# Performance work log

Hardware: AMD Instinct MI355X
Metric: run time of the kernel (lower is better)

The kernel has to match this reference:

```python
import jax, jax.numpy as jnp
import numpy as np

B, S, NS, MAX_W, H, NH = 4, 512, 8192, 16, 256, 4
DH = H // NH
FF = 4 * H
NEG = -1e9  # finite mask value; fully-padded spans are zeroed at the end anyway


def _layernorm(x, g, b, eps=1e-5):
    m = jnp.mean(x, -1, keepdims=True)
    v = jnp.var(x, -1, keepdims=True)
    return (x - m) * jax.lax.rsqrt(v + eps) * g + b


def _pos_encoding(n, d):
    pos = np.arange(n)[:, None]
    div = np.exp(np.arange(0, d, 2) * (-np.log(10000.0) / d))
    pe = np.zeros((n, d), np.float32)
    pe[:, 0::2] = np.sin(pos * div)
    pe[:, 1::2] = np.cos(pos * div)
    return jnp.asarray(pe)


def setup_inputs():
    key = jax.random.key(0)
    ks = jax.random.split(key, 12)
    sc = 1.0 / np.sqrt(H)
    starts = jax.random.randint(ks[1], (B, NS), 0, S - MAX_W)
    lengths = jax.random.randint(ks[2], (B, NS), 1, MAX_W + 1)
    return {
        "token_reps": jax.random.normal(ks[0], (B, S, H), jnp.float32),
        "span_ids": jnp.stack([starts, starts + lengths], -1),
        "span_masks": jax.random.uniform(ks[3], (B, NS)) < 0.9,
        "pooling": 1,
        "dummy_query": jax.random.normal(ks[4], (H,), jnp.float32) * sc,
        "w_q": jax.random.normal(ks[5], (H, H), jnp.float32) * sc,
        "w_k": jax.random.normal(ks[6], (H, H), jnp.float32) * sc,
        "w_v": jax.random.normal(ks[7], (H, H), jnp.float32) * sc,
        "b_qkv": jnp.zeros((3, H), jnp.float32),
        "w_o": jax.random.normal(ks[8], (H, H), jnp.float32) * sc,
        "b_o": jnp.zeros((H,), jnp.float32),
        "ln_g": jnp.ones((H,), jnp.float32),
        "ln_b": jnp.zeros((H,), jnp.float32),
        "ffn_w1": jax.random.normal(ks[9], (H, FF), jnp.float32) * sc,
        "ffn_b1": jnp.zeros((FF,), jnp.float32),
        "ffn_w2": jax.random.normal(ks[10], (FF, H), jnp.float32) * (1.0 / np.sqrt(FF)),
        "ffn_b2": jnp.zeros((H,), jnp.float32),
    }


def reference(token_reps, span_ids, span_masks, pooling, dummy_query, w_q, w_k, w_v,
              b_qkv, w_o, b_o, ln_g, ln_b, ffn_w1, ffn_b1, ffn_w2, ffn_b2):
    # sequence positional encoding (eval mode -> dropout is identity)
    tr = token_reps + _pos_encoding(S, H)[None]  # [B,S,H]
    # span lengths, zeroed where span is masked out (as in torch code)
    span_len = (span_ids[:, :, 1] - span_ids[:, :, 0]) * span_masks.astype(span_ids.dtype)  # [B,NS]
    offs = jnp.arange(MAX_W)
    valid = offs[None, None, :] < span_len[:, :, None]  # [B,NS,W] True = real token
    pos = jnp.clip(span_ids[:, :, 0:1] + offs[None, None, :], 0, S - 1)  # [B,NS,W]
    # vectorized ragged gather replacing the python double loop
    x = tr[jnp.arange(B)[:, None, None], pos]  # [B,NS,W,H]
    x = jnp.where(valid[..., None], x, 0.0)
    # single-query multi-head cross attention (dummy query attends over span tokens)
    q = (dummy_query @ w_q.T + b_qkv[0]).reshape(NH, DH)
    k = (x @ w_k.T + b_qkv[1]).reshape(B, NS, MAX_W, NH, DH)
    v = (x @ w_v.T + b_qkv[2]).reshape(B, NS, MAX_W, NH, DH)
    logits = jnp.einsum('hd,bnwhd->bnhw', q, k) / np.sqrt(DH)
    logits = jnp.where(valid[:, :, None, :], logits, NEG)
    attn = jax.nn.softmax(logits, axis=-1)
    ctx = jnp.einsum('bnhw,bnwhd->bnhd', attn, v).reshape(B, NS, H)
    out = ctx @ w_o.T + b_o + dummy_query  # residual with the dummy query
    y = _layernorm(out, ln_g, ln_b)
    f = jax.nn.relu(y @ ffn_w1 + ffn_b1) @ ffn_w2 + ffn_b2
    y = _layernorm(f + y, ln_g, ln_b)
    return jnp.where(span_masks[..., None], y, 0.0)  # [B,NS,H]
```

## Files before the change

kernel.cpp:

```cpp
#include <hip/hip_runtime.h>
#include <hip/hip_bf16.h>

#define B_    4
#define S_    512
#define NS_   8192
#define MAXW  16
#define H_    256
#define NH_   4
#define DH_   64
#define FF_   1024
#define NSPAN (B_*NS_)
#define NEGV  (-1.0e9f)
#define MT    64

typedef short s16x8 __attribute__((ext_vector_type(8)));
typedef float f32x4 __attribute__((ext_vector_type(4)));

__device__ __forceinline__ unsigned short f2bu(float v){
  __hip_bfloat16 h = __float2bfloat16(v);
  union { __hip_bfloat16 h; unsigned short u; } c; c.h = h; return c.u;
}
__device__ __forceinline__ float bu2f(unsigned short u){
  union { unsigned int i; float f; } c; c.i = ((unsigned int)u) << 16; return c.f;
}

__global__ void prep_tr_kernel(const float* __restrict__ tok,
                               float* __restrict__ tr,
                               unsigned short* __restrict__ trbf){
  int idx = blockIdx.x * 256 + threadIdx.x;
  int j = idx & (H_ - 1);
  int p = (idx >> 8) & (S_ - 1);
  float fac = expf((float)((j >> 1) * 2) * (-9.210340371976184f / 256.0f));
  float ang = (float)p * fac;
  float pe = (j & 1) ? cosf(ang) : sinf(ang);
  float v = tok[idx] + pe;
  tr[idx] = v;
  trbf[idx] = f2bu(v);
}

__global__ void prep_q_kernel(const float* __restrict__ dq,
                              const float* __restrict__ wq,
                              const float* __restrict__ wk,
                              const float* __restrict__ bqkv,
                              float* __restrict__ qkvec,
                              float* __restrict__ qb){
  __shared__ float q_s[H_];
  const int t = threadIdx.x;
  const int l = t & 63;
  const int wv = t >> 6;
  const int h = blockIdx.x;
  float4 dqv = *(const float4*)(dq + l*4);
  for (int r = 0; r < 64; ++r) {
    const int row = wv*64 + r;
    float4 wr = *(const float4*)(wq + (size_t)row*H_ + l*4);
    float p = wr.x*dqv.x + wr.y*dqv.y + wr.z*dqv.z + wr.w*dqv.w;
    p += __shfl_xor(p, 1);  p += __shfl_xor(p, 2);
    p += __shfl_xor(p, 4);  p += __shfl_xor(p, 8);
    p += __shfl_xor(p, 16); p += __shfl_xor(p, 32);
    if (l == 0) q_s[row] = p + bqkv[row];
  }
  __syncthreads();
  float s = 0.f;
  #pragma unroll 8
  for (int d = 0; d < DH_; ++d) s += q_s[h*DH_ + d] * wk[(h*DH_ + d)*H_ + t];
  qkvec[h*H_ + t] = s;
  if (t < 64) {
    float p = q_s[h*DH_ + t] * bqkv[H_ + h*DH_ + t];
    for (int off = 32; off; off >>= 1) p += __shfl_down(p, off);
    if (t == 0) qb[h] = p;
  }
}

__global__ __launch_bounds__(256) void prep_logit_kernel(
    const float* __restrict__ tr, const float* __restrict__ qkvec,
    const float* __restrict__ qb, float* __restrict__ lt)
{
  const int t = threadIdx.x, l = t & 63, wv = t >> 6;
  const int row = blockIdx.x * 4 + wv;
  float4 x = *(const float4*)(tr + (size_t)row*H_ + l*4);
  float p0, p1, p2, p3;
  {
    float4 q0 = *(const float4*)(qkvec + 0*H_ + l*4);
    float4 q1 = *(const float4*)(qkvec + 1*H_ + l*4);
    float4 q2 = *(const float4*)(qkvec + 2*H_ + l*4);
    float4 q3 = *(const float4*)(qkvec + 3*H_ + l*4);
    p0 = q0.x*x.x + q0.y*x.y + q0.z*x.z + q0.w*x.w;
    p1 = q1.x*x.x + q1.y*x.y + q1.z*x.z + q1.w*x.w;
    p2 = q2.x*x.x + q2.y*x.y + q2.z*x.z + q2.w*x.w;
    p3 = q3.x*x.x + q3.y*x.y + q3.z*x.z + q3.w*x.w;
  }
  #pragma unroll
  for (int m = 1; m < 64; m <<= 1) {
    p0 += __shfl_xor(p0, m); p1 += __shfl_xor(p1, m);
    p2 += __shfl_xor(p2, m); p3 += __shfl_xor(p3, m);
  }
  if (l < 4) {
    float pv = (l == 0) ? p0 : (l == 1) ? p1 : (l == 2) ? p2 : p3;
    lt[row*NH_ + l] = (pv + qb[l]) * 0.125f;
  }
}

__global__ void cast_bf16_kernel(const float* __restrict__ src,
                                 unsigned short* __restrict__ dst){
  int idx = blockIdx.x * 256 + threadIdx.x;
  dst[idx] = f2bu(src[idx]);
}

__global__ void prep_w1t_kernel(const float* __restrict__ w1,
                                unsigned short* __restrict__ w1t){
  int idx = blockIdx.x * 256 + threadIdx.x;
  int n = idx >> 8, k = idx & 255;
  w1t[idx] = f2bu(w1[k*FF_ + n]);
}
__global__ void prep_w2t_kernel(const float* __restrict__ w2,
                                unsigned short* __restrict__ w2t){
  int idx = blockIdx.x * 256 + threadIdx.x;
  int n = idx >> 10, k = idx & 1023;
  w2t[idx] = f2bu(w2[k*H_ + n]);
}

__global__ __launch_bounds__(256) void pool_kernel(
    const unsigned short* __restrict__ trbf,
    const float* __restrict__ lt,
    const int* __restrict__ span_ids, const int* __restrict__ span_masks,
    int span0, unsigned short* __restrict__ pooled)
{
  const int t = threadIdx.x;
  const int l = t & 63;
  const int wv = t >> 6;
  const int spanL = blockIdx.x * 4 + wv;
  const int span  = span0 + spanL;
  const int b  = span >> 13;
  const int st = span_ids[span*2];
  const int en = span_ids[span*2 + 1];
  const int len = span_masks[span] ? (en - st) : 0;

  const int h = l >> 4, w = l & 15;
  int pos = st + w; pos = pos < 0 ? 0 : (pos > S_-1 ? S_-1 : pos);
  float logit = (w < len) ? lt[(b*S_ + pos)*NH_ + h] : NEGV;
  float mx = logit;
  mx = fmaxf(mx, __shfl_xor(mx, 1));
  mx = fmaxf(mx, __shfl_xor(mx, 2));
  mx = fmaxf(mx, __shfl_xor(mx, 4));
  mx = fmaxf(mx, __shfl_xor(mx, 8));
  float e = expf(logit - mx);
  float se = e;
  se += __shfl_xor(se, 1); se += __shfl_xor(se, 2);
  se += __shfl_xor(se, 4); se += __shfl_xor(se, 8);
  const float av = e / se;

  float acc[NH_][4];
  #pragma unroll
  for (int hh = 0; hh < NH_; ++hh)
    #pragma unroll
    for (int j = 0; j < 4; ++j) acc[hh][j] = 0.f;

  const unsigned short* rb = trbf + (size_t)(b*S_)*H_ + l*4;
  #pragma unroll
  for (int w2 = 0; w2 < MAXW; ++w2) {
    int p2 = st + w2; p2 = p2 < 0 ? 0 : (p2 > S_-1 ? S_-1 : p2);
    ushort4 xv = *(const ushort4*)(rb + (size_t)p2*H_);
    float x0 = bu2f(xv.x), x1 = bu2f(xv.y), x2 = bu2f(xv.z), x3 = bu2f(xv.w);
    #pragma unroll
    for (int hh = 0; hh < NH_; ++hh) {
      float a = __shfl(av, hh*16 + w2);
      acc[hh][0] += a*x0; acc[hh][1] += a*x1;
      acc[hh][2] += a*x2; acc[hh][3] += a*x3;
    }
  }
  unsigned short* pp = pooled + (size_t)spanL * 1024;
  #pragma unroll
  for (int hh = 0; hh < NH_; ++hh) {
    ushort4 o;
    o.x = f2bu(acc[hh][0]); o.y = f2bu(acc[hh][1]);
    o.z = f2bu(acc[hh][2]); o.w = f2bu(acc[hh][3]);
    *(ushort4*)(pp + hh*256 + l*4) = o;
  }
}

template <typename AF>
__device__ __forceinline__ void do_gemm(AF aload, const unsigned short* __restrict__ bmat,
                                        int bstr, int koff, f32x4 (&ac)[4][4],
                                        int w, int ln16, int lg)
{
  s16x8 BA[4], BB[4];
  const unsigned short* bb = bmat + koff + lg*8;
  #pragma unroll
  for (int nf = 0; nf < 4; ++nf) {
    const unsigned short* bp = bb + (size_t)(w*64 + nf*16 + ln16)*bstr;
    BA[nf] = *(const s16x8*)bp;
    BB[nf] = *(const s16x8*)(bp + 32);
  }
  #pragma unroll
  for (int kk = 0; kk < 4; ++kk) {
    const int k0 = kk*64;
    {
      s16x8 a0 = aload(0*16 + ln16, k0 + lg*8);
      s16x8 a1 = aload(1*16 + ln16, k0 + lg*8);
      s16x8 a2 = aload(2*16 + ln16, k0 + lg*8);
      s16x8 a3 = aload(3*16 + ln16, k0 + lg*8);
      #pragma unroll
      for (int nf = 0; nf < 4; ++nf) {
        ac[0][nf] = __builtin_amdgcn_mfma_f32_16x16x32_bf16(a0, BA[nf], ac[0][nf], 0,0,0);
        ac[1][nf] = __builtin_amdgcn_mfma_f32_16x16x32_bf16(a1, BA[nf], ac[1][nf], 0,0,0);
        ac[2][nf] = __builtin_amdgcn_mfma_f32_16x16x32_bf16(a2, BA[nf], ac[2][nf], 0,0,0);
        ac[3][nf] = __builtin_amdgcn_mfma_f32_16x16x32_bf16(a3, BA[nf], ac[3][nf], 0,0,0);
      }
    }
    if (kk < 3) {
      #pragma unroll
      for (int nf = 0; nf < 4; ++nf)
        BA[nf] = *(const s16x8*)(bb + (size_t)(w*64 + nf*16 + ln16)*bstr + k0 + 64);
    }
    {
      s16x8 a0 = aload(0*16 + ln16, k0 + 32 + lg*8);
      s16x8 a1 = aload(1*16 + ln16, k0 + 32 + lg*8);
      s16x8 a2 = aload(2*16 + ln16, k0 + 32 + lg*8);
      s16x8 a3 = aload(3*16 + ln16, k0 + 32 + lg*8);
      #pragma unroll
      for (int nf = 0; nf < 4; ++nf) {
        ac[0][nf] = __builtin_amdgcn_mfma_f32_16x16x32_bf16(a0, BB[nf], ac[0][nf], 0,0,0);
        ac[1][nf] = __builtin_amdgcn_mfma_f32_16x16x32_bf16(a1, BB[nf], ac[1][nf], 0,0,0);
        ac[2][nf] = __builtin_amdgcn_mfma_f32_16x16x32_bf16(a2, BB[nf], ac[2][nf], 0,0,0);
        ac[3][nf] = __builtin_amdgcn_mfma_f32_16x16x32_bf16(a3, BB[nf], ac[3][nf], 0,0,0);
      }
    }
    if (kk < 3) {
      #pragma unroll
      for (int nf = 0; nf < 4; ++nf)
        BB[nf] = *(const s16x8*)(bb + (size_t)(w*64 + nf*16 + ln16)*bstr + k0 + 96);
    }
  }
}

__global__ __launch_bounds__(256) void fused_gemm_kernel(
    const unsigned short* __restrict__ pooled,
    const unsigned short* __restrict__ wvt,
    const unsigned short* __restrict__ wot,
    const float* __restrict__ bqkv, const float* __restrict__ bo,
    const float* __restrict__ dq,
    const unsigned short* __restrict__ w1t, const float* __restrict__ b1,
    const unsigned short* __restrict__ w2t, const float* __restrict__ b2,
    const float* __restrict__ lng, const float* __restrict__ lnb,
    const int* __restrict__ masks, int span0,
    float* __restrict__ out)
{
  __shared__ __align__(16) unsigned short buf_s[MT][264];
  __shared__ __align__(16) unsigned short y_s[MT][264];
  __shared__ float part_s[4][MT][2];

  const int t = threadIdx.x;
  const int l = t & 63;
  const int w = t >> 6;
  const int ln16 = l & 15;
  const int lg = l >> 4;
  const int m0l = blockIdx.x * MT;
  const int m0g = span0 + m0l;

  auto aldP = [&](int r, int kc) -> s16x8 {
    return *(const s16x8*)(pooled + (size_t)(m0l + r)*1024 + w*256 + kc);
  };
  auto aldY = [&](int r, int kc) -> s16x8 { return *(const s16x8*)&y_s[r][kc]; };
  auto aldB = [&](int r, int kc) -> s16x8 { return *(const s16x8*)&buf_s[r][kc]; };

  f32x4 acc[4][4];

  #pragma unroll
  for (int mf = 0; mf < 4; ++mf)
    #pragma unroll
    for (int nf = 0; nf < 4; ++nf) acc[mf][nf] = (f32x4){0.f,0.f,0.f,0.f};
  do_gemm(aldP, wvt, 256, 0, acc, w, ln16, lg);
  #pragma unroll
  for (int nf = 0; nf < 4; ++nf) {
    const int col = w*64 + nf*16 + ln16;
    const float bvv = bqkv[2*H_ + col];
    #pragma unroll
    for (int mf = 0; mf < 4; ++mf)
      #pragma unroll
      for (int r = 0; r < 4; ++r)
        buf_s[mf*16 + lg*4 + r][col] = f2bu(acc[mf][nf][r] + bvv);
  }
  __syncthreads();

  #pragma unroll
  for (int mf = 0; mf < 4; ++mf)
    #pragma unroll
    for (int nf = 0; nf < 4; ++nf) acc[mf][nf] = (f32x4){0.f,0.f,0.f,0.f};
  do_gemm(aldB, wot, 256, 0, acc, w, ln16, lg);

  {
    float bbv[4], glv[4], blv[4];
    #pragma unroll
    for (int nf = 0; nf < 4; ++nf) {
      const int col = w*64 + nf*16 + ln16;
      bbv[nf] = bo[col] + dq[col];
      glv[nf] = lng[col]; blv[nf] = lnb[col];
    }
    float vals[4][4][4];
    #pragma unroll
    for (int mf = 0; mf < 4; ++mf)
      #pragma unroll
      for (int r = 0; r < 4; ++r) {
        const int row = mf*16 + lg*4 + r;
        float s1 = 0.f, s2 = 0.f;
        #pragma unroll
        for (int nf = 0; nf < 4; ++nf) {
          float v = acc[mf][nf][r] + bbv[nf];
          vals[mf][r][nf] = v; s1 += v; s2 += v*v;
        }
        s1 += __shfl_xor(s1,1); s2 += __shfl_xor(s2,1);
        s1 += __shfl_xor(s1,2); s2 += __shfl_xor(s2,2);
        s1 += __shfl_xor(s1,4); s2 += __shfl_xor(s2,4);
        s1 += __shfl_xor(s1,8); s2 += __shfl_xor(s2,8);
        if (ln16 == 0) { part_s[w][row][0] = s1; part_s[w][row][1] = s2; }
      }
    __syncthreads();
    #pragma unroll
    for (int mf = 0; mf < 4; ++mf)
      #pragma unroll
      for (int r = 0; r < 4; ++r) {
        const int row = mf*16 + lg*4 + r;
        float s1 = part_s[0][row][0]+part_s[1][row][0]+part_s[2][row][0]+part_s[3][row][0];
        float s2 = part_s[0][row][1]+part_s[1][row][1]+part_s[2][row][1]+part_s[3][row][1];
        float mean = s1 * (1.f/H_);
        float var  = s2 * (1.f/H_) - mean*mean; var = fmaxf(var, 0.f);
        float rstd = rsqrtf(var + 1e-5f);
        #pragma unroll
        for (int nf = 0; nf < 4; ++nf) {
          const int col = w*64 + nf*16 + ln16;
          y_s[row][col] = f2bu((vals[mf][r][nf] - mean)*rstd*glv[nf] + blv[nf]);
        }
      }
  }
  __syncthreads();

  f32x4 f2acc[4][4];
  #pragma unroll
  for (int mf = 0; mf < 4; ++mf)
    #pragma unroll
    for (int nf = 0; nf < 4; ++nf) f2acc[mf][nf] = (f32x4){0.f,0.f,0.f,0.f};

  for (int nc = 0; nc < 4; ++nc) {
    #pragma unroll
    for (int mf = 0; mf < 4; ++mf)
      #pragma unroll
      for (int nf = 0; nf < 4; ++nf) acc[mf][nf] = (f32x4){0.f,0.f,0.f,0.f};
    do_gemm(aldY, w1t + nc*256*H_, 256, 0, acc, w, ln16, lg);
    __syncthreads();
    #pragma unroll
    for (int nf = 0; nf < 4; ++nf) {
      float bb = b1[nc*256 + w*64 + nf*16 + ln16];
      #pragma unroll
      for (int mf = 0; mf < 4; ++mf)
        #pragma unroll
        for (int r = 0; r < 4; ++r)
          buf_s[mf*16 + lg*4 + r][w*64 + nf*16 + ln16] = f2bu(fmaxf(acc[mf][nf][r] + bb, 0.f));
    }
    __syncthreads();
    do_gemm(aldB, w2t, 1024, nc*256, f2acc, w, ln16, lg);
  }

  float b2v[4], gv[4], bvv[4];
  #pragma unroll
  for (int nf = 0; nf < 4; ++nf) {
    const int col = w*64 + nf*16 + ln16;
    b2v[nf] = b2[col]; gv[nf] = lng[col]; bvv[nf] = lnb[col];
  }
  float vals[4][4][4];
  #pragma unroll
  for (int mf = 0; mf < 4; ++mf)
    #pragma unroll
    for (int r = 0; r < 4; ++r) {
      const int row = mf*16 + lg*4 + r;
      float s1 = 0.f, s2 = 0.f;
      #pragma unroll
      for (int nf = 0; nf < 4; ++nf) {
        float resid = bu2f(y_s[row][w*64 + nf*16 + ln16]);
        float v = f2acc[mf][nf][r] + b2v[nf] + resid;
        vals[mf][r][nf] = v; s1 += v; s2 += v*v;
      }
      s1 += __shfl_xor(s1,1); s2 += __shfl_xor(s2,1);
      s1 += __shfl_xor(s1,2); s2 += __shfl_xor(s2,2);
      s1 += __shfl_xor(s1,4); s2 += __shfl_xor(s2,4);
      s1 += __shfl_xor(s1,8); s2 += __shfl_xor(s2,8);
      if (ln16 == 0) { part_s[w][row][0] = s1; part_s[w][row][1] = s2; }
    }
  __syncthreads();
  #pragma unroll
  for (int mf = 0; mf < 4; ++mf)
    #pragma unroll
    for (int r = 0; r < 4; ++r) {
      const int row = mf*16 + lg*4 + r;
      const int span = m0g + row;
      float s1 = part_s[0][row][0]+part_s[1][row][0]+part_s[2][row][0]+part_s[3][row][0];
      float s2 = part_s[0][row][1]+part_s[1][row][1]+part_s[2][row][1]+part_s[3][row][1];
      float mean = s1 * (1.f/H_);
      float var  = s2 * (1.f/H_) - mean*mean; var = fmaxf(var, 0.f);
      float rstd = rsqrtf(var + 1e-5f);
      int mk = masks[span];
      #pragma unroll
      for (int nf = 0; nf < 4; ++nf) {
        const int col = w*64 + nf*16 + ln16;
        float yv = (vals[mf][r][nf] - mean)*rstd*gv[nf] + bvv[nf];
        out[(size_t)span*H_ + col] = mk ? yv : 0.f;
      }
    }
}

extern "C" void kernel_launch(void* const* d_in, const int* in_sizes, int n_in,
                              void* d_out, int out_size, void* d_ws, size_t ws_size,
                              hipStream_t stream) {
  const float* tok      = (const float*)d_in[0];
  const int* span_ids   = (const int*)d_in[1];
  const int* span_masks = (const int*)d_in[2];
  const float* dq   = (const float*)d_in[4];
  const float* wq   = (const float*)d_in[5];
  const float* wk   = (const float*)d_in[6];
  const float* wv   = (const float*)d_in[7];
  const float* bqkv = (const float*)d_in[8];
  const float* wo   = (const float*)d_in[9];
  const float* bo   = (const float*)d_in[10];
  const float* lng  = (const float*)d_in[11];
  const float* lnb  = (const float*)d_in[12];
  const float* w1   = (const float*)d_in[13];
  const float* b1   = (const float*)d_in[14];
  const float* w2   = (const float*)d_in[15];
  const float* b2   = (const float*)d_in[16];

  float* ws    = (float*)d_ws;
  float* tr    = ws;
  float* qkvec = ws + 524288;
  float* qbuf  = qkvec + 1024;
  float* lt    = qbuf + 8;
  unsigned short* ub = (unsigned short*)(lt + 8192);
  unsigned short* trbf   = ub;
  unsigned short* wvt    = trbf + 524288;
  unsigned short* wot    = wvt + 65536;
  unsigned short* w1t    = wot + 65536;
  unsigned short* w2t    = w1t + 262144;
  unsigned short* pooled = w2t + 262144;

  const size_t fixed_bytes = (size_t)(524288 + 1024 + 8 + 8192)*4
                           + (size_t)(524288 + 65536*2 + 262144*2)*2;
  int nb = 1;
  while (nb < 16 && fixed_bytes + (size_t)(NSPAN/nb)*1024*2 > ws_size) nb <<= 1;
  const int spans_b = NSPAN / nb;

  hipLaunchKernelGGL(prep_tr_kernel, dim3(B_*S_*H_/256), dim3(256), 0, stream, tok, tr, trbf);
  hipLaunchKernelGGL(prep_q_kernel, dim3(NH_), dim3(256), 0, stream,
                     dq, wq, wk, bqkv, qkvec, qbuf);
  hipLaunchKernelGGL(prep_logit_kernel, dim3(B_*S_/4), dim3(256), 0, stream,
                     tr, qkvec, qbuf, lt);
  hipLaunchKernelGGL(cast_bf16_kernel, dim3(65536/256), dim3(256), 0, stream, wv, wvt);
  hipLaunchKernelGGL(cast_bf16_kernel, dim3(65536/256), dim3(256), 0, stream, wo, wot);
  hipLaunchKernelGGL(prep_w1t_kernel, dim3(262144/256), dim3(256), 0, stream, w1, w1t);
  hipLaunchKernelGGL(prep_w2t_kernel, dim3(262144/256), dim3(256), 0, stream, w2, w2t);

  for (int bi = 0; bi < nb; ++bi) {
    const int span0 = bi * spans_b;
    hipLaunchKernelGGL(pool_kernel, dim3(spans_b/4), dim3(256), 0, stream,
                       trbf, lt, span_ids, span_masks, span0, pooled);
    hipLaunchKernelGGL(fused_gemm_kernel, dim3(spans_b/MT), dim3(256), 0, stream,
                       pooled, wvt, wot, bqkv, bo, dq, w1t, b1, w2t, b2,
                       lng, lnb, span_masks, span0, (float*)d_out);
  }
}
```

Baseline: 218.4 us.

## Fold V and O projections into one combined weight and widen GEMM block to 8 waves

Precomputes a combined per-head weight Wo·Wv (256x1024, bf16) plus a folded bias, so the pooled per-head activations go through one K=1024 GEMM instead of a V projection followed by an O projection. The fused kernel now runs 512 threads (8 waves, 32 columns each), streams the pooled tile through double-buffered LDS, and prefetches B fragments. This removes one intermediate GEMM and its LDS round trip. In exchange the first GEMM has K=1024 instead of two K=256 GEMMs, so it does more MFMA work, and the combined weight adds an extra bf16 rounding step.

New measurement: 247.0 us. +13.1%, slower.

```diff
diff --git a/kernel.cpp b/kernel.cpp
--- a/kernel.cpp
+++ b/kernel.cpp
@@ -7,11 +7,11 @@
 #define MAXW  16
 #define H_    256
 #define NH_   4
-#define DH_   64
 #define FF_   1024
 #define NSPAN (B_*NS_)
 #define NEGV  (-1.0e9f)
 #define MT    64
+#define LDSK  264
 
 typedef short s16x8 __attribute__((ext_vector_type(8)));
 typedef float f32x4 __attribute__((ext_vector_type(4)));
@@ -22,6 +22,9 @@
 }
 __device__ __forceinline__ float bu2f(unsigned short u){
   union { unsigned int i; float f; } c; c.i = ((unsigned int)u) << 16; return c.f;
+}
+__device__ __forceinline__ f32x4 MFMA(s16x8 a, s16x8 b, f32x4 c){
+  return __builtin_amdgcn_mfma_f32_16x16x32_bf16(a, b, c, 0, 0, 0);
 }
 
 __global__ void prep_tr_kernel(const float* __restrict__ tok,
@@ -62,10 +65,10 @@
   __syncthreads();
   float s = 0.f;
   #pragma unroll 8
-  for (int d = 0; d < DH_; ++d) s += q_s[h*DH_ + d] * wk[(h*DH_ + d)*H_ + t];
+  for (int d = 0; d < 64; ++d) s += q_s[h*64 + d] * wk[(h*64 + d)*H_ + t];
   qkvec[h*H_ + t] = s;
   if (t < 64) {
-    float p = q_s[h*DH_ + t] * bqkv[H_ + h*DH_ + t];
+    float p = q_s[h*64 + t] * bqkv[H_ + h*64 + t];
     for (int off = 32; off; off >>= 1) p += __shfl_down(p, off);
     if (t == 0) qb[h] = p;
   }
@@ -100,23 +103,54 @@
   }
 }
 
-__global__ void cast_bf16_kernel(const float* __restrict__ src,
-                                 unsigned short* __restrict__ dst){
-  int idx = blockIdx.x * 256 + threadIdx.x;
-  dst[idx] = f2bu(src[idx]);
+__global__ __launch_bounds__(256) void prep_wcomb_kernel(
+    const float* __restrict__ wv, const float* __restrict__ wo,
+    unsigned short* __restrict__ wct)
+{
+  __shared__ float wo_s[H_];
+  const int i = blockIdx.x;
+  const int t = threadIdx.x;
+  wo_s[t] = wo[(size_t)i*H_ + t];
+  __syncthreads();
+  #pragma unroll
+  for (int h = 0; h < NH_; ++h) {
+    float s = 0.f;
+    #pragma unroll 8
+    for (int d = 0; d < 64; ++d)
+      s += wo_s[h*64 + d] * wv[(size_t)(h*64 + d)*H_ + t];
+    wct[(size_t)i*1024 + h*H_ + t] = f2bu(s);
+  }
+}
+
+__global__ void prep_zbias_kernel(const float* __restrict__ wo,
+                                  const float* __restrict__ bqkv,
+                                  const float* __restrict__ bo,
+                                  const float* __restrict__ dq,
+                                  float* __restrict__ zb){
+  const int t = threadIdx.x, l = t & 63, wv = t >> 6;
+  float4 bv4 = *(const float4*)(bqkv + 2*H_ + l*4);
+  for (int r = 0; r < 64; ++r) {
+    int row = wv*64 + r;
+    float4 wr = *(const float4*)(wo + (size_t)row*H_ + l*4);
+    float p = wr.x*bv4.x + wr.y*bv4.y + wr.z*bv4.z + wr.w*bv4.w;
+    p += __shfl_xor(p, 1);  p += __shfl_xor(p, 2);
+    p += __shfl_xor(p, 4);  p += __shfl_xor(p, 8);
+    p += __shfl_xor(p, 16); p += __shfl_xor(p, 32);
+    if (l == 0) zb[row] = p + bo[row] + dq[row];
+  }
 }
 
 __global__ void prep_w1t_kernel(const float* __restrict__ w1,
                                 unsigned short* __restrict__ w1t){
   int idx = blockIdx.x * 256 + threadIdx.x;
   int n = idx >> 8, k = idx & 255;
-  w1t[idx] = f2bu(w1[k*FF_ + n]);
+  w1t[idx] = f2bu(w1[(size_t)k*FF_ + n]);
 }
 __global__ void prep_w2t_kernel(const float* __restrict__ w2,
                                 unsigned short* __restrict__ w2t){
   int idx = blockIdx.x * 256 + threadIdx.x;
   int n = idx >> 10, k = idx & 1023;
-  w2t[idx] = f2bu(w2[k*H_ + n]);
+  w2t[idx] = f2bu(w2[(size_t)k*H_ + n]);
 }
 
 __global__ __launch_bounds__(256) void pool_kernel(
@@ -178,76 +212,42 @@
   }
 }
 
-template <typename AF>
-__device__ __forceinline__ void do_gemm(AF aload, const unsigned short* __restrict__ bmat,
-                                        int bstr, int koff, f32x4 (&ac)[4][4],
-                                        int w, int ln16, int lg)
+__device__ __forceinline__ void gemm8(const unsigned short* __restrict__ As,
+                                      const unsigned short* __restrict__ bp0,
+                                      const unsigned short* __restrict__ bp1,
+                                      f32x4 (&ac)[4][2], int ln16, int lg)
 {
-  s16x8 BA[4], BB[4];
-  const unsigned short* bb = bmat + koff + lg*8;
-  #pragma unroll
-  for (int nf = 0; nf < 4; ++nf) {
-    const unsigned short* bp = bb + (size_t)(w*64 + nf*16 + ln16)*bstr;
-    BA[nf] = *(const s16x8*)bp;
-    BB[nf] = *(const s16x8*)(bp + 32);
-  }
-  #pragma unroll
-  for (int kk = 0; kk < 4; ++kk) {
-    const int k0 = kk*64;
-    {
-      s16x8 a0 = aload(0*16 + ln16, k0 + lg*8);
-      s16x8 a1 = aload(1*16 + ln16, k0 + lg*8);
-      s16x8 a2 = aload(2*16 + ln16, k0 + lg*8);
-      s16x8 a3 = aload(3*16 + ln16, k0 + lg*8);
-      #pragma unroll
-      for (int nf = 0; nf < 4; ++nf) {
-        ac[0][nf] = __builtin_amdgcn_mfma_f32_16x16x32_bf16(a0, BA[nf], ac[0][nf], 0,0,0);
-        ac[1][nf] = __builtin_amdgcn_mfma_f32_16x16x32_bf16(a1, BA[nf], ac[1][nf], 0,0,0);
-        ac[2][nf] = __builtin_amdgcn_mfma_f32_16x16x32_bf16(a2, BA[nf], ac[2][nf], 0,0,0);
-        ac[3][nf] = __builtin_amdgcn_mfma_f32_16x16x32_bf16(a3, BA[nf], ac[3][nf], 0,0,0);
-      }
-    }
-    if (kk < 3) {
-      #pragma unroll
-      for (int nf = 0; nf < 4; ++nf)
-        BA[nf] = *(const s16x8*)(bb + (size_t)(w*64 + nf*16 + ln16)*bstr + k0 + 64);
-    }
-    {
-      s16x8 a0 = aload(0*16 + ln16, k0 + 32 + lg*8);
-      s16x8 a1 = aload(1*16 + ln16, k0 + 32 + lg*8);
-      s16x8 a2 = aload(2*16 + ln16, k0 + 32 + lg*8);
-      s16x8 a3 = aload(3*16 + ln16, k0 + 32 + lg*8);
-      #pragma unroll
-      for (int nf = 0; nf < 4; ++nf) {
-        ac[0][nf] = __builtin_amdgcn_mfma_f32_16x16x32_bf16(a0, BB[nf], ac[0][nf], 0,0,0);
-        ac[1][nf] = __builtin_amdgcn_mfma_f32_16x16x32_bf16(a1, BB[nf], ac[1][nf], 0,0,0);
-        ac[2][nf] = __builtin_amdgcn_mfma_f32_16x16x32_bf16(a2, BB[nf], ac[2][nf], 0,0,0);
-        ac[3][nf] = __builtin_amdgcn_mfma_f32_16x16x32_bf16(a3, BB[nf], ac[3][nf], 0,0,0);
-      }
-    }
-    if (kk < 3) {
-      #pragma unroll
-      for (int nf = 0; nf < 4; ++nf)
-        BB[nf] = *(const s16x8*)(bb + (size_t)(w*64 + nf*16 + ln16)*bstr + k0 + 96);
-    }
-  }
-}
-
-__global__ __launch_bounds__(256) void fused_gemm_kernel(
+  s16x8 B0 = *(const s16x8*)bp0;
+  s16x8 B1 = *(const s16x8*)bp1;
+  #pragma unroll
+  for (int s = 0; s < 8; ++s) {
+    s16x8 N0 = B0, N1 = B1;
+    if (s < 7) { N0 = *(const s16x8*)(bp0 + (s+1)*32); N1 = *(const s16x8*)(bp1 + (s+1)*32); }
+    s16x8 a0 = *(const s16x8*)(As + (0*16+ln16)*LDSK + s*32 + lg*8);
+    s16x8 a1 = *(const s16x8*)(As + (1*16+ln16)*LDSK + s*32 + lg*8);
+    s16x8 a2 = *(const s16x8*)(As + (2*16+ln16)*LDSK + s*32 + lg*8);
+    s16x8 a3 = *(const s16x8*)(As + (3*16+ln16)*LDSK + s*32 + lg*8);
+    ac[0][0]=MFMA(a0,B0,ac[0][0]); ac[1][0]=MFMA(a1,B0,ac[1][0]);
+    ac[2][0]=MFMA(a2,B0,ac[2][0]); ac[3][0]=MFMA(a3,B0,ac[3][0]);
+    ac[0][1]=MFMA(a0,B1,ac[0][1]); ac[1][1]=MFMA(a1,B1,ac[1][1]);
+    ac[2][1]=MFMA(a2,B1,ac[2][1]); ac[3][1]=MFMA(a3,B1,ac[3][1]);
+    B0 = N0; B1 = N1;
+  }
+}
+
+__global__ __launch_bounds__(512, 4) void fused_gemm_kernel(
     const unsigned short* __restrict__ pooled,
-    const unsigned short* __restrict__ wvt,
-    const unsigned short* __restrict__ wot,
-    const float* __restrict__ bqkv, const float* __restrict__ bo,
-    const float* __restrict__ dq,
+    const unsigned short* __restrict__ wct,
+    const float* __restrict__ zbias,
     const unsigned short* __restrict__ w1t, const float* __restrict__ b1,
     const unsigned short* __restrict__ w2t, const float* __restrict__ b2,
     const float* __restrict__ lng, const float* __restrict__ lnb,
     const int* __restrict__ masks, int span0,
     float* __restrict__ out)
 {
-  __shared__ __align__(16) unsigned short buf_s[MT][264];
-  __shared__ __align__(16) unsigned short y_s[MT][264];
-  __shared__ float part_s[4][MT][2];
+  __shared__ __align__(16) unsigned short bufA[MT][LDSK];
+  __shared__ __align__(16) unsigned short bufB[MT][LDSK];
+  __shared__ float part_s[8][MT][2];
 
   const int t = threadIdx.x;
   const int l = t & 63;
@@ -256,58 +256,96 @@
   const int lg = l >> 4;
   const int m0l = blockIdx.x * MT;
   const int m0g = span0 + m0l;
-
-  auto aldP = [&](int r, int kc) -> s16x8 {
-    return *(const s16x8*)(pooled + (size_t)(m0l + r)*1024 + w*256 + kc);
+  const int ncol = w * 32;
+
+  int srow[4], k8[4];
+  #pragma unroll
+  for (int q = 0; q < 4; ++q) {
+    int idx = q*512 + t;
+    srow[q] = idx >> 5;
+    k8[q]   = (idx & 31)*8;
+  }
+  const unsigned short* pbase = pooled + (size_t)m0l*1024;
+
+  f32x4 acc[4][2];
+  #pragma unroll
+  for (int mf = 0; mf < 4; ++mf){ acc[mf][0]=(f32x4){0,0,0,0}; acc[mf][1]=(f32x4){0,0,0,0}; }
+
+  const unsigned short* bz0 = wct + (size_t)(ncol + ln16)*1024 + lg*8;
+  const unsigned short* bz1 = wct + (size_t)(ncol + 16 + ln16)*1024 + lg*8;
+
+  unsigned short* As = &bufA[0][0];
+  unsigned short* An = &bufB[0][0];
+
+  uint4 sr[4];
+  #pragma unroll
+  for (int q = 0; q < 4; ++q)
+    sr[q] = *(const uint4*)(pbase + (size_t)srow[q]*1024 + k8[q]);
+  #pragma unroll
+  for (int q = 0; q < 4; ++q)
+    *(uint4*)(As + srow[q]*LDSK + k8[q]) = sr[q];
+  __syncthreads();
+
+  s16x8 GA[4], GB[4];
+  #define LOADBZ(G, kkg) { \
+    G[0] = *(const s16x8*)(bz0 + (kkg)*64);      \
+    G[1] = *(const s16x8*)(bz0 + (kkg)*64 + 32); \
+    G[2] = *(const s16x8*)(bz1 + (kkg)*64);      \
+    G[3] = *(const s16x8*)(bz1 + (kkg)*64 + 32); }
+  LOADBZ(GA, 0); LOADBZ(GB, 1);
+
+  auto zstep = [&](s16x8 (&G)[4], int kk, int kkgnext) {
+    #pragma unroll
+    for (int half = 0; half < 2; ++half) {
+      s16x8 a0 = *(const s16x8*)(As + (0*16+ln16)*LDSK + kk*64 + half*32 + lg*8);
+      s16x8 a1 = *(const s16x8*)(As + (1*16+ln16)*LDSK + kk*64 + half*32 + lg*8);
+      s16x8 a2 = *(const s16x8*)(As + (2*16+ln16)*LDSK + kk*64 + half*32 + lg*8);
+      s16x8 a3 = *(const s16x8*)(As + (3*16+ln16)*LDSK + kk*64 + half*32 + lg*8);
+      acc[0][0]=MFMA(a0,G[0+half],acc[0][0]); acc[1][0]=MFMA(a1,G[0+half],acc[1][0]);
+      acc[2][0]=MFMA(a2,G[0+half],acc[2][0]); acc[3][0]=MFMA(a3,G[0+half],acc[3][0]);
+      acc[0][1]=MFMA(a0,G[2+half],acc[0][1]); acc[1][1]=MFMA(a1,G[2+half],acc[1][1]);
+      acc[2][1]=MFMA(a2,G[2+half],acc[2][1]); acc[3][1]=MFMA(a3,G[2+half],acc[3][1]);
+    }
+    if (kkgnext < 16) LOADBZ(G, kkgnext);
   };
-  auto aldY = [&](int r, int kc) -> s16x8 { return *(const s16x8*)&y_s[r][kc]; };
-  auto aldB = [&](int r, int kc) -> s16x8 { return *(const s16x8*)&buf_s[r][kc]; };
-
-  f32x4 acc[4][4];
-
-  #pragma unroll
-  for (int mf = 0; mf < 4; ++mf)
-    #pragma unroll
-    for (int nf = 0; nf < 4; ++nf) acc[mf][nf] = (f32x4){0.f,0.f,0.f,0.f};
-  do_gemm(aldP, wvt, 256, 0, acc, w, ln16, lg);
-  #pragma unroll
-  for (int nf = 0; nf < 4; ++nf) {
-    const int col = w*64 + nf*16 + ln16;
-    const float bvv = bqkv[2*H_ + col];
-    #pragma unroll
-    for (int mf = 0; mf < 4; ++mf)
-      #pragma unroll
-      for (int r = 0; r < 4; ++r)
-        buf_s[mf*16 + lg*4 + r][col] = f2bu(acc[mf][nf][r] + bvv);
-  }
-  __syncthreads();
-
-  #pragma unroll
-  for (int mf = 0; mf < 4; ++mf)
-    #pragma unroll
-    for (int nf = 0; nf < 4; ++nf) acc[mf][nf] = (f32x4){0.f,0.f,0.f,0.f};
-  do_gemm(aldB, wot, 256, 0, acc, w, ln16, lg);
-
+
+  #pragma unroll
+  for (int c = 0; c < 4; ++c) {
+    if (c < 3) {
+      #pragma unroll
+      for (int q = 0; q < 4; ++q)
+        sr[q] = *(const uint4*)(pbase + (size_t)srow[q]*1024 + (c+1)*256 + k8[q]);
+    }
+    zstep(GA, 0, c*4 + 2);
+    zstep(GB, 1, c*4 + 3);
+    zstep(GA, 2, c*4 + 4);
+    zstep(GB, 3, c*4 + 5);
+    if (c < 3) {
+      #pragma unroll
+      for (int q = 0; q < 4; ++q)
+        *(uint4*)(An + srow[q]*LDSK + k8[q]) = sr[q];
+      __syncthreads();
+      unsigned short* tmp = As; As = An; An = tmp;
+    }
+  }
+  #undef LOADBZ
+
+  unsigned short* y_s  = &bufB[0][0];
+  unsigned short* f1_s = &bufA[0][0];
   {
-    float bbv[4], glv[4], blv[4];
-    #pragma unroll
-    for (int nf = 0; nf < 4; ++nf) {
-      const int col = w*64 + nf*16 + ln16;
-      bbv[nf] = bo[col] + dq[col];
-      glv[nf] = lng[col]; blv[nf] = lnb[col];
-    }
-    float vals[4][4][4];
+    const float zb0 = zbias[ncol + ln16],      zb1 = zbias[ncol + 16 + ln16];
+    const float g0  = lng[ncol + ln16],        g1  = lng[ncol + 16 + ln16];
+    const float bl0 = lnb[ncol + ln16],        bl1 = lnb[ncol + 16 + ln16];
+    float vals[4][4][2];
     #pragma unroll
     for (int mf = 0; mf < 4; ++mf)
       #pragma unroll
       for (int r = 0; r < 4; ++r) {
         const int row = mf*16 + lg*4 + r;
-        float s1 = 0.f, s2 = 0.f;
-        #pragma unroll
-        for (int nf = 0; nf < 4; ++nf) {
-          float v = acc[mf][nf][r] + bbv[nf];
-          vals[mf][r][nf] = v; s1 += v; s2 += v*v;
-        }
+        float v0 = acc[mf][0][r] + zb0;
+        float v1 = acc[mf][1][r] + zb1;
+        vals[mf][r][0] = v0; vals[mf][r][1] = v1;
+        float s1 = v0 + v1, s2 = v0*v0 + v1*v1;
         s1 += __shfl_xor(s1,1); s2 += __shfl_xor(s2,1);
         s1 += __shfl_xor(s1,2); s2 += __shfl_xor(s2,2);
         s1 += __shfl_xor(s1,4); s2 += __shfl_xor(s2,4);
@@ -320,91 +358,88 @@
       #pragma unroll
       for (int r = 0; r < 4; ++r) {
         const int row = mf*16 + lg*4 + r;
-        float s1 = part_s[0][row][0]+part_s[1][row][0]+part_s[2][row][0]+part_s[3][row][0];
-        float s2 = part_s[0][row][1]+part_s[1][row][1]+part_s[2][row][1]+part_s[3][row][1];
+        float s1 = 0.f, s2 = 0.f;
+        #pragma unroll
+        for (int j = 0; j < 8; ++j) { s1 += part_s[j][row][0]; s2 += part_s[j][row][1]; }
         float mean = s1 * (1.f/H_);
         float var  = s2 * (1.f/H_) - mean*mean; var = fmaxf(var, 0.f);
         float rstd = rsqrtf(var + 1e-5f);
-        #pragma unroll
-        for (int nf = 0; nf < 4; ++nf) {
-          const int col = w*64 + nf*16 + ln16;
-          y_s[row][col] = f2bu((vals[mf][r][nf] - mean)*rstd*glv[nf] + blv[nf]);
-        }
+        y_s[row*LDSK + ncol + ln16]      = f2bu((vals[mf][r][0]-mean)*rstd*g0 + bl0);
+        y_s[row*LDSK + ncol + 16 + ln16] = f2bu((vals[mf][r][1]-mean)*rstd*g1 + bl1);
       }
   }
   __syncthreads();
 
-  f32x4 f2acc[4][4];
-  #pragma unroll
-  for (int mf = 0; mf < 4; ++mf)
-    #pragma unroll
-    for (int nf = 0; nf < 4; ++nf) f2acc[mf][nf] = (f32x4){0.f,0.f,0.f,0.f};
-
+  f32x4 f2acc[4][2];
+  #pragma unroll
+  for (int mf = 0; mf < 4; ++mf){ f2acc[mf][0]=(f32x4){0,0,0,0}; f2acc[mf][1]=(f32x4){0,0,0,0}; }
+
+  #pragma unroll 1
   for (int nc = 0; nc < 4; ++nc) {
     #pragma unroll
-    for (int mf = 0; mf < 4; ++mf)
-      #pragma unroll
-      for (int nf = 0; nf < 4; ++nf) acc[mf][nf] = (f32x4){0.f,0.f,0.f,0.f};
-    do_gemm(aldY, w1t + nc*256*H_, 256, 0, acc, w, ln16, lg);
+    for (int mf = 0; mf < 4; ++mf){ acc[mf][0]=(f32x4){0,0,0,0}; acc[mf][1]=(f32x4){0,0,0,0}; }
+    const unsigned short* b10 = w1t + (size_t)(nc*256 + ncol + ln16)*256 + lg*8;
+    const unsigned short* b11 = w1t + (size_t)(nc*256 + ncol + 16 + ln16)*256 + lg*8;
+    gemm8(y_s, b10, b11, acc, ln16, lg);
     __syncthreads();
-    #pragma unroll
-    for (int nf = 0; nf < 4; ++nf) {
-      float bb = b1[nc*256 + w*64 + nf*16 + ln16];
+    {
+      const float bb0 = b1[nc*256 + ncol + ln16];
+      const float bb1 = b1[nc*256 + ncol + 16 + ln16];
       #pragma unroll
       for (int mf = 0; mf < 4; ++mf)
         #pragma unroll
-        for (int r = 0; r < 4; ++r)
-          buf_s[mf*16 + lg*4 + r][w*64 + nf*16 + ln16] = f2bu(fmaxf(acc[mf][nf][r] + bb, 0.f));
+        for (int r = 0; r < 4; ++r) {
+          const int row = mf*16 + lg*4 + r;
+          f1_s[row*LDSK + ncol + ln16]      = f2bu(fmaxf(acc[mf][0][r] + bb0, 0.f));
+          f1_s[row*LDSK + ncol + 16 + ln16] = f2bu(fmaxf(acc[mf][1][r] + bb1, 0.f));
+        }
     }
     __syncthreads();
-    do_gemm(aldB, w2t, 1024, nc*256, f2acc, w, ln16, lg);
-  }
-
-  float b2v[4], gv[4], bvv[4];
-  #pragma unroll
-  for (int nf = 0; nf < 4; ++nf) {
-    const int col = w*64 + nf*16 + ln16;
-    b2v[nf] = b2[col]; gv[nf] = lng[col]; bvv[nf] = lnb[col];
-  }
-  float vals[4][4][4];
-  #pragma unroll
-  for (int mf = 0; mf < 4; ++mf)
-    #pragma unroll
-    for (int r = 0; r < 4; ++r) {
-      const int row = mf*16 + lg*4 + r;
-      float s1 = 0.f, s2 = 0.f;
-      #pragma unroll
-      for (int nf = 0; nf < 4; ++nf) {
-        float resid = bu2f(y_s[row][w*64 + nf*16 + ln16]);
-        float v = f2acc[mf][nf][r] + b2v[nf] + resid;
-        vals[mf][r][nf] = v; s1 += v; s2 += v*v;
+    const unsigned short* b20 = w2t + (size_t)(ncol + ln16)*1024 + nc*256 + lg*8;
+    const unsigned short* b21 = w2t + (size_t)(ncol + 16 + ln16)*1024 + nc*256 + lg*8;
+    gemm8(f1_s, b20, b21, f2acc, ln16, lg);
+  }
+
+  {
+    const float b20v = b2[ncol + ln16],   b21v = b2[ncol + 16 + ln16];
+    const float g0   = lng[ncol + ln16],  g1   = lng[ncol + 16 + ln16];
+    const float bl0  = lnb[ncol + ln16],  bl1  = lnb[ncol + 16 + ln16];
+    float vals[4][4][2];
+    #pragma unroll
+    for (int mf = 0; mf < 4; ++mf)
+      #pragma unroll
+      for (int r = 0; r < 4; ++r) {
+        const int row = mf*16 + lg*4 + r;
+        float v0 = f2acc[mf][0][r] + b20v + bu2f(y_s[row*LDSK + ncol + ln16]);
+        float v1 = f2acc[mf][1][r] + b21v + bu2f(y_s[row*LDSK + ncol + 16 + ln16]);
+        vals[mf][r][0] = v0; vals[mf][r][1] = v1;
+        float s1 = v0 + v1, s2 = v0*v0 + v1*v1;
+        s1 += __shfl_xor(s1,1); s2 += __shfl_xor(s2,1);
+        s1 += __shfl_xor(s1,2); s2 += __shfl_xor(s2,2);
+        s1 += __shfl_xor(s1,4); s2 += __shfl_xor(s2,4);
+        s1 += __shfl_xor(s1,8); s2 += __shfl_xor(s2,8);
+        if (ln16 == 0) { part_s[w][row][0] = s1; part_s[w][row][1] = s2; }
       }
-      s1 += __shfl_xor(s1,1); s2 += __shfl_xor(s2,1);
-      s1 += __shfl_xor(s1,2); s2 += __shfl_xor(s2,2);
-      s1 += __shfl_xor(s1,4); s2 += __shfl_xor(s2,4);
-      s1 += __shfl_xor(s1,8); s2 += __shfl_xor(s2,8);
-      if (ln16 == 0) { part_s[w][row][0] = s1; part_s[w][row][1] = s2; }
-    }
-  __syncthreads();
-  #pragma unroll
-  for (int mf = 0; mf < 4; ++mf)
-    #pragma unroll
-    for (int r = 0; r < 4; ++r) {
-      const int row = mf*16 + lg*4 + r;
-      const int span = m0g + row;
-      float s1 = part_s[0][row][0]+part_s[1][row][0]+part_s[2][row][0]+part_s[3][row][0];
-      float s2 = part_s[0][row][1]+part_s[1][row][1]+part_s[2][row][1]+part_s[3][row][1];
-      float mean = s1 * (1.f/H_);
-      float var  = s2 * (1.f/H_) - mean*mean; var = fmaxf(var, 0.f);
-      float rstd = rsqrtf(var + 1e-5f);
-      int mk = masks[span];
-      #pragma unroll
-      for (int nf = 0; nf < 4; ++nf) {
-        const int col = w*64 + nf*16 + ln16;
-        float yv = (vals[mf][r][nf] - mean)*rstd*gv[nf] + bvv[nf];
-        out[(size_t)span*H_ + col] = mk ? yv : 0.f;
+    __syncthreads();
+    #pragma unroll
+    for (int mf = 0; mf < 4; ++mf)
+      #pragma unroll
+      for (int r = 0; r < 4; ++r) {
+        const int row = mf*16 + lg*4 + r;
+        const int span = m0g + row;
+        float s1 = 0.f, s2 = 0.f;
+        #pragma unroll
+        for (int j = 0; j < 8; ++j) { s1 += part_s[j][row][0]; s2 += part_s[j][row][1]; }
+        float mean = s1 * (1.f/H_);
+        float var  = s2 * (1.f/H_) - mean*mean; var = fmaxf(var, 0.f);
+        float rstd = rsqrtf(var + 1e-5f);
+        int mk = masks[span];
+        float o0 = (vals[mf][r][0]-mean)*rstd*g0 + bl0;
+        float o1 = (vals[mf][r][1]-mean)*rstd*g1 + bl1;
+        out[(size_t)span*H_ + ncol + ln16]      = mk ? o0 : 0.f;
+        out[(size_t)span*H_ + ncol + 16 + ln16] = mk ? o1 : 0.f;
       }
-    }
+  }
 }
 
 extern "C" void kernel_launch(void* const* d_in, const int* in_sizes, int n_in,
@@ -432,16 +467,16 @@
   float* qkvec = ws + 524288;
   float* qbuf  = qkvec + 1024;
   float* lt    = qbuf + 8;
-  unsigned short* ub = (unsigned short*)(lt + 8192);
+  float* zbias = lt + 8192;
+  unsigned short* ub = (unsigned short*)(zbias + 256);
   unsigned short* trbf   = ub;
-  unsigned short* wvt    = trbf + 524288;
-  unsigned short* wot    = wvt + 65536;
-  unsigned short* w1t    = wot + 65536;
+  unsigned short* wct    = trbf + 524288;
+  unsigned short* w1t    = wct + 262144;
   unsigned short* w2t    = w1t + 262144;
   unsigned short* pooled = w2t + 262144;
 
-  const size_t fixed_bytes = (size_t)(524288 + 1024 + 8 + 8192)*4
-                           + (size_t)(524288 + 65536*2 + 262144*2)*2;
+  const size_t fixed_bytes = (size_t)(524288 + 1024 + 8 + 8192 + 256)*4
+                           + (size_t)(524288 + 262144*3)*2;
   int nb = 1;
   while (nb < 16 && fixed_bytes + (size_t)(NSPAN/nb)*1024*2 > ws_size) nb <<= 1;
   const int spans_b = NSPAN / nb;
@@ -451,8 +486,9 @@
                      dq, wq, wk, bqkv, qkvec, qbuf);
   hipLaunchKernelGGL(prep_logit_kernel, dim3(B_*S_/4), dim3(256), 0, stream,
                      tr, qkvec, qbuf, lt);
-  hipLaunchKernelGGL(cast_bf16_kernel, dim3(65536/256), dim3(256), 0, stream, wv, wvt);
-  hipLaunchKernelGGL(cast_bf16_kernel, dim3(65536/256), dim3(256), 0, stream, wo, wot);
+  hipLaunchKernelGGL(prep_wcomb_kernel, dim3(H_), dim3(256), 0, stream, wv, wo, wct);
+  hipLaunchKernelGGL(prep_zbias_kernel, dim3(1), dim3(256), 0, stream,
+                     wo, bqkv, bo, dq, zbias);
   hipLaunchKernelGGL(prep_w1t_kernel, dim3(262144/256), dim3(256), 0, stream, w1, w1t);
   hipLaunchKernelGGL(prep_w2t_kernel, dim3(262144/256), dim3(256), 0, stream, w2, w2t);
 
@@ -460,8 +496,8 @@
     const int span0 = bi * spans_b;
     hipLaunchKernelGGL(pool_kernel, dim3(spans_b/4), dim3(256), 0, stream,
                        trbf, lt, span_ids, span_masks, span0, pooled);
-    hipLaunchKernelGGL(fused_gemm_kernel, dim3(spans_b/MT), dim3(256), 0, stream,
-                       pooled, wvt, wot, bqkv, bo, dq, w1t, b1, w2t, b2,
+    hipLaunchKernelGGL(fused_gemm_kernel, dim3(spans_b/MT), dim3(512), 0, stream,
+                       pooled, wct, zbias, w1t, b1, w2t, b2,
                        lng, lnb, span_masks, span0, (float*)d_out);
   }
 }
```
